# Optimization experiments

Measured on AMD Instinct MI355X. Metric: run time of the kernel, lower is better.

The kernel has to match this reference:

```python
import jax, jax.numpy as jnp
import numpy as np

N_NODES = 100000
N_EDGES = 1600000
DIM = 128
HEADS = 8
PHC = DIM // HEADS  # per-head channels = 16


def setup_inputs() -> dict:
    key = jax.random.key(0)
    k1, k2, k3, k4, k5 = jax.random.split(key, 5)
    nodes = jax.random.normal(k1, (N_NODES, DIM), dtype=jnp.float32)
    senders = jax.random.randint(k2, (N_EDGES,), 0, N_NODES, dtype=jnp.int32)
    receivers = jax.random.randint(k3, (N_EDGES,), 0, N_NODES, dtype=jnp.int32)
    # VarianceScaling(fan_avg, uniform) ~ limit = sqrt(3/fan_avg)
    lim_w = np.sqrt(3.0 / DIM)
    W = jax.random.uniform(k4, (DIM, DIM), minval=-lim_w, maxval=lim_w, dtype=jnp.float32)
    b = jnp.zeros((DIM,), dtype=jnp.float32)
    lim_a = np.sqrt(3.0 * 2.0 / (2 * PHC + 1))
    attn_w = jax.random.uniform(k5, (2 * PHC, 1), minval=-lim_a, maxval=lim_a, dtype=jnp.float32)
    attn_b = jnp.zeros((1,), dtype=jnp.float32)
    return {"nodes": nodes, "senders": senders, "receivers": receivers,
            "W": W, "b": b, "attn_w": attn_w, "attn_b": attn_b}


def reference(nodes, senders, receivers, W, b, attn_w, attn_b):
    n = nodes.shape[0]
    # linear transform + split heads: [N, H, PHC]
    nt = (nodes @ W + b).reshape(n, HEADS, PHC)
    sent = nt[senders]      # [E, H, PHC] gather
    recv = nt[receivers]    # [E, H, PHC] gather
    # attention logits: Linear(1) over leaky_relu(concat(q,k)) -> [E, H, 1]
    qk = jax.nn.leaky_relu(jnp.concatenate([sent, recv], axis=-1), negative_slope=0.2)
    logits = qk @ attn_w + attn_b  # [E, H, 1]
    # segment softmax over edges grouped by receiver node
    seg_max = jax.ops.segment_max(logits, receivers, num_segments=n)  # [N, H, 1]
    exp = jnp.exp(logits - seg_max[receivers])
    denom = jax.ops.segment_sum(exp, receivers, num_segments=n)  # [N, H, 1]
    alpha = exp / denom[receivers]
    # weighted scatter-sum of sender features
    out = jax.ops.segment_sum(sent * alpha, receivers, num_segments=n)  # [N, H, PHC]
    return out.reshape(n, -1)  # concat=True -> [N, DIM]
```

## Files before the change

### kernel.cpp

```cpp
#include <hip/hip_runtime.h>

#define DIM 128
#define HEADS 8
#define PHC 16

#define BSHIFT 6
#define BNODES 64
#define CAP 1408
#define NBMAX 1600

typedef __bf16 bf16x4 __attribute__((ext_vector_type(4)));
typedef __bf16 bf16x8 __attribute__((ext_vector_type(8)));
typedef float  f32x4  __attribute__((ext_vector_type(4)));

__device__ inline unsigned short f2bf(float x) {
  unsigned int u = __float_as_uint(x);
  unsigned int r = (u + 0x7FFF + ((u >> 16) & 1)) >> 16;
  return (unsigned short)r;
}

__global__ __launch_bounds__(256) void k_prepw(
    const float* __restrict__ W, __bf16* __restrict__ Wh,
    __bf16* __restrict__ Wl, int* __restrict__ gCursor, int NB) {
  const int tuple = blockIdx.x * 256 + threadIdx.x;
  if (tuple < NB) gCursor[tuple] = 0;
  const int ln = tuple & 15;
  const int lg = (tuple >> 4) & 3;
  const int cg = (tuple >> 6) & 7;
  const int kt = tuple >> 9;
  const int col = (cg << 4) + ln;
  bf16x8 h, l;
#pragma unroll
  for (int e = 0; e < 8; ++e) {
    int k = (kt << 5) + ((e >> 2) << 4) + (lg << 2) + (e & 3);
    float wv = W[k * DIM + col];
    __bf16 hh = (__bf16)wv;
    h[e] = hh;
    l[e] = (__bf16)(wv - (float)hh);
  }
  *(bf16x8*)(Wh + tuple * 8) = h;
  *(bf16x8*)(Wl + tuple * 8) = l;
}

#define GROWS 64

__global__ __launch_bounds__(256, 3) void k_gemm_scatter(
    const float* __restrict__ A, const __bf16* __restrict__ Wh,
    const __bf16* __restrict__ Wl, const float* __restrict__ bias,
    const float* __restrict__ attn_w, unsigned int* __restrict__ nt_t,
    float* __restrict__ s_exp_t, const int* __restrict__ send,
    const int* __restrict__ recv, int* __restrict__ gCursor,
    unsigned int* __restrict__ pairs, int E, int NB, int nScat, int n) {
  __shared__ __align__(16) float smemF[GROWS * DIM];

  if (blockIdx.x < nScat) {
    int* cnt = (int*)smemF;
    int* cur = cnt + NBMAX;
    const int t = threadIdx.x;
    for (int i = t; i < NB; i += 256) cnt[i] = 0;
    __syncthreads();
    const int e0 = blockIdx.x * 8192;
    const int e1 = min(e0 + 8192, E);
    for (int i = e0 + t; i < e1; i += 256)
      atomicAdd(&cnt[recv[i] >> BSHIFT], 1);
    __syncthreads();
    for (int i = t; i < NB; i += 256) {
      int c = cnt[i];
      cur[i] = i * CAP + (c ? atomicAdd(&gCursor[i], c) : 0);
    }
    __syncthreads();
    for (int i = e0 + t; i < e1; i += 256) {
      int r = recv[i];
      int b = r >> BSHIFT;
      int p = atomicAdd(&cur[b], 1);
      if (p - b * CAP < CAP)
        pairs[p] = (unsigned int)send[i] | ((unsigned int)(r & (BNODES - 1)) << 17);
    }
    return;
  }

  __bf16* Ah = (__bf16*)smemF;
  __bf16* Al = Ah + GROWS * DIM;
  const int t    = threadIdx.x;
  const int row0 = (blockIdx.x - nScat) * GROWS;
  const int lane = t & 63;
  const int w    = t >> 6;
  const int lg   = lane >> 4;
  const int ln   = lane & 15;

  float4 av[8];
  {
    const float4* A4 = (const float4*)(A + (size_t)row0 * DIM);
    const int lim = min(GROWS, n - row0) * (DIM / 4);
#pragma unroll
    for (int j = 0; j < 8; ++j) {
      int i = t + j * 256;
      av[j] = (i < lim) ? A4[i] : make_float4(0.f, 0.f, 0.f, 0.f);
    }
  }

#pragma unroll
  for (int j = 0; j < 8; ++j) {
    int i = t + j * 256;
    int r = i >> 5, c4 = i & 31;
    int ktc = c4 >> 3, lgc = c4 & 3, ehi = (c4 >> 2) & 1;
    int unit = (r << 4) + (((ktc << 2) + lgc) ^ (r & 15));
    int ei = (unit << 3) + (ehi << 2);
    float x0 = av[j].x, x1 = av[j].y, x2 = av[j].z, x3 = av[j].w;
    __bf16 h0 = (__bf16)x0, h1 = (__bf16)x1, h2 = (__bf16)x2, h3 = (__bf16)x3;
    bf16x4 hv = {h0, h1, h2, h3};
    bf16x4 lv = {(__bf16)(x0 - (float)h0), (__bf16)(x1 - (float)h1),
                 (__bf16)(x2 - (float)h2), (__bf16)(x3 - (float)h3)};
    *(bf16x4*)(Ah + ei) = hv;
    *(bf16x4*)(Al + ei) = lv;
  }

  f32x4 acc[4][2];
  {
    const float b0 = bias[(w << 5) + ln];
    const float b1 = bias[(w << 5) + 16 + ln];
#pragma unroll
    for (int rt = 0; rt < 4; ++rt) {
      acc[rt][0] = (f32x4){b0, b0, b0, b0};
      acc[rt][1] = (f32x4){b1, b1, b1, b1};
    }
  }
  __syncthreads();

  const int cg0 = w << 1;
#pragma unroll
  for (int kt = 0; kt < 4; ++kt) {
    bf16x8 Bh0, Bl0, Bh1, Bl1;
    {
      int i0 = ((((kt << 3) + cg0) << 2) + lg) * 16 + ln;
      int i1 = ((((kt << 3) + cg0 + 1) << 2) + lg) * 16 + ln;
      Bh0 = *(const bf16x8*)(Wh + (i0 << 3));
      Bl0 = *(const bf16x8*)(Wl + (i0 << 3));
      Bh1 = *(const bf16x8*)(Wh + (i1 << 3));
      Bl1 = *(const bf16x8*)(Wl + (i1 << 3));
    }
    bf16x8 ah[4], al[4];
#pragma unroll
    for (int rt = 0; rt < 4; ++rt) {
      int m = (rt << 4) + ln;
      int u = (m << 4) + (((kt << 2) + lg) ^ (m & 15));
      ah[rt] = *(const bf16x8*)(Ah + (u << 3));
      al[rt] = *(const bf16x8*)(Al + (u << 3));
    }
#pragma unroll
    for (int rt = 0; rt < 4; ++rt) {
      acc[rt][0] = __builtin_amdgcn_mfma_f32_16x16x32_bf16(ah[rt], Bh0, acc[rt][0], 0, 0, 0);
      acc[rt][0] = __builtin_amdgcn_mfma_f32_16x16x32_bf16(ah[rt], Bl0, acc[rt][0], 0, 0, 0);
      acc[rt][0] = __builtin_amdgcn_mfma_f32_16x16x32_bf16(al[rt], Bh0, acc[rt][0], 0, 0, 0);
      acc[rt][1] = __builtin_amdgcn_mfma_f32_16x16x32_bf16(ah[rt], Bh1, acc[rt][1], 0, 0, 0);
      acc[rt][1] = __builtin_amdgcn_mfma_f32_16x16x32_bf16(ah[rt], Bl1, acc[rt][1], 0, 0, 0);
      acc[rt][1] = __builtin_amdgcn_mfma_f32_16x16x32_bf16(al[rt], Bh1, acc[rt][1], 0, 0, 0);
    }
  }

  __syncthreads();

#pragma unroll
  for (int rt = 0; rt < 4; ++rt)
#pragma unroll
    for (int ct = 0; ct < 2; ++ct) {
      int colx = ((w << 5) + (ct << 4) + ln) ^ ((lg & 1) << 4);
#pragma unroll
      for (int r = 0; r < 4; ++r) {
        int rowl = (rt << 4) + (lg << 2) + r;
        smemF[(rowl << 7) + colx] = acc[rt][ct][r];
      }
    }

  {
    const float aw = attn_w[ln];
#pragma unroll
    for (int rt = 0; rt < 4; ++rt)
#pragma unroll
      for (int ct = 0; ct < 2; ++ct) {
        const int head = (w << 1) + ct;
#pragma unroll
        for (int r = 0; r < 4; ++r) {
          float v = acc[rt][ct][r];
          float p = (v > 0.f ? v : 0.2f * v) * aw;
          p += __shfl_xor(p, 1);
          p += __shfl_xor(p, 2);
          p += __shfl_xor(p, 4);
          p += __shfl_xor(p, 8);
          if (ln == 0) {
            int row = row0 + (rt << 4) + (lg << 2) + r;
            if (row < n) s_exp_t[(size_t)head * n + row] = __expf(p);
          }
        }
      }
  }
  __syncthreads();

  {
    const int nrow = min(GROWS, n - row0);
    const int r = t >> 2;
    const int q = t & 3;
    if (r < nrow) {
#pragma unroll
      for (int j = 0; j < 8; ++j) {
        int c4 = (j << 2) + q;
        int c4s = c4 ^ (((r >> 2) & 1) << 2);
        f32x4 v = *(const f32x4*)(smemF + (r << 7) + (c4s << 2));
        unsigned int lo = (unsigned int)f2bf(v[0]) | ((unsigned int)f2bf(v[1]) << 16);
        unsigned int hi = (unsigned int)f2bf(v[2]) | ((unsigned int)f2bf(v[3]) << 16);
        ((uint2*)nt_t)[((size_t)j * n + row0 + r) * 4 + q] = make_uint2(lo, hi);
      }
    }
  }
}

__global__ __launch_bounds__(256) void k_aggbuild(
    const unsigned int* __restrict__ pairs, const int* __restrict__ gCursor,
    const unsigned int* __restrict__ nt_t, const float* __restrict__ s_exp_t,
    float* __restrict__ out, int n) {
  __shared__ unsigned int buf[CAP];
  __shared__ int csr_l[CAP];
  __shared__ int hist[BNODES], offl[BNODES], curl[BNODES];
  const int b = blockIdx.x >> 3;
  const int h = blockIdx.x & 7;
  const int t = threadIdx.x;
  const int base = b * CAP;
  const int bsize = min(gCursor[b], CAP);

  for (int i = t; i < bsize; i += 256)
    buf[i] = __builtin_nontemporal_load(&pairs[base + i]);
  if (t < BNODES) hist[t] = 0;
  __syncthreads();
  for (int i = t; i < bsize; i += 256)
    atomicAdd(&hist[(buf[i] >> 17) & (BNODES - 1)], 1);
  __syncthreads();
  if (t < 64) {
    int v = hist[t];
    int x = v;
#pragma unroll
    for (int off = 1; off < 64; off <<= 1) {
      int y = __shfl_up(x, off);
      if (t >= off) x += y;
    }
    offl[t] = x - v;
    curl[t] = x - v;
  }
  __syncthreads();
  for (int i = t; i < bsize; i += 256) {
    unsigned int v = buf[i];
    int p = atomicAdd(&curl[(v >> 17) & (BNODES - 1)], 1);
    csr_l[p] = (int)(v & 0x1FFFF);
  }
  __syncthreads();

  const int nl = t >> 2;
  const int q  = t & 3;
  const int node = (b << BSHIFT) + nl;
  const int deg = hist[nl];
  const int eoff = offl[nl];
  const uint2* nt2 = (const uint2*)nt_t;
  const float* sp = s_exp_t + (size_t)h * n;
  const size_t pb4 = (size_t)h * n * 4;

  f32x4 a = {0.f, 0.f, 0.f, 0.f};
  float den = 0.f;
  for (int j = 0; j < deg; j += 4) {
    bool ok1 = (j + 1) < deg, ok2 = (j + 2) < deg, ok3 = (j + 3) < deg;
    int s0 = csr_l[eoff + j];
    int s1 = csr_l[ok1 ? (eoff + j + 1) : eoff];
    int s2 = csr_l[ok2 ? (eoff + j + 2) : eoff];
    int s3 = csr_l[ok3 ? (eoff + j + 3) : eoff];
    float w0 = sp[s0];
    float w1 = ok1 ? sp[s1] : 0.f;
    float w2 = ok2 ? sp[s2] : 0.f;
    float w3 = ok3 ? sp[s3] : 0.f;
    uint2 q0 = nt2[pb4 + s0 * 4 + q];
    uint2 q1 = nt2[pb4 + s1 * 4 + q];
    uint2 q2 = nt2[pb4 + s2 * 4 + q];
    uint2 q3 = nt2[pb4 + s3 * 4 + q];
    den += (w0 + w1) + (w2 + w3);
    a.x = fmaf(w0, __uint_as_float(q0.x << 16),
          fmaf(w1, __uint_as_float(q1.x << 16),
          fmaf(w2, __uint_as_float(q2.x << 16),
          fmaf(w3, __uint_as_float(q3.x << 16), a.x))));
    a.y = fmaf(w0, __uint_as_float(q0.x & 0xFFFF0000u),
          fmaf(w1, __uint_as_float(q1.x & 0xFFFF0000u),
          fmaf(w2, __uint_as_float(q2.x & 0xFFFF0000u),
          fmaf(w3, __uint_as_float(q3.x & 0xFFFF0000u), a.y))));
    a.z = fmaf(w0, __uint_as_float(q0.y << 16),
          fmaf(w1, __uint_as_float(q1.y << 16),
          fmaf(w2, __uint_as_float(q2.y << 16),
          fmaf(w3, __uint_as_float(q3.y << 16), a.z))));
    a.w = fmaf(w0, __uint_as_float(q0.y & 0xFFFF0000u),
          fmaf(w1, __uint_as_float(q1.y & 0xFFFF0000u),
          fmaf(w2, __uint_as_float(q2.y & 0xFFFF0000u),
          fmaf(w3, __uint_as_float(q3.y & 0xFFFF0000u), a.w))));
  }
  if (node < n) {
    const float inv = (deg > 0) ? 1.0f / den : 0.f;
    f32x4 o = {a.x * inv, a.y * inv, a.z * inv, a.w * inv};
    __builtin_nontemporal_store(
        o, (f32x4*)out + (size_t)node * 32 + (h << 2) + q);
  }
}

extern "C" void kernel_launch(void* const* d_in, const int* in_sizes, int n_in,
                              void* d_out, int out_size, void* d_ws, size_t ws_size,
                              hipStream_t stream) {
  const float* nodes   = (const float*)d_in[0];
  const int*   senders = (const int*)d_in[1];
  const int*   recvs   = (const int*)d_in[2];
  const float* W       = (const float*)d_in[3];
  const float* bias    = (const float*)d_in[4];
  const float* attn_w  = (const float*)d_in[5];

  const int n = in_sizes[0] / DIM;
  const int E = in_sizes[1];
  const int NB = (n + BNODES - 1) >> BSHIFT;

  char* w = (char*)d_ws;
  auto align256 = [](size_t x) { return (x + 255) & ~(size_t)255; };
  size_t off = 0;
  unsigned int* nt_t = (unsigned int*)(w + off); off += align256((size_t)n * DIM * 2);
  float* s_exp_t = (float*)(w + off); off += align256((size_t)n * HEADS * 4);
  unsigned int* pairs = (unsigned int*)(w + off); off += align256((size_t)NB * CAP * 4);
  int* gCursor   = (int*)(w + off);   off += align256((size_t)NB * 4);
  __bf16* Wh     = (__bf16*)(w + off); off += align256((size_t)2048 * 8 * 2);
  __bf16* Wl     = (__bf16*)(w + off); off += align256((size_t)2048 * 8 * 2);
  (void)ws_size;

  k_prepw<<<8, 256, 0, stream>>>(W, Wh, Wl, gCursor, NB);
  const int nScat = (E + 8191) / 8192;
  const int ngemm = (n + GROWS - 1) / GROWS;
  k_gemm_scatter<<<nScat + ngemm, 256, 0, stream>>>(
      nodes, Wh, Wl, bias, attn_w, nt_t, s_exp_t,
      senders, recvs, gCursor, pairs, E, NB, nScat, n);
  k_aggbuild<<<NB * 8, 256, 0, stream>>>(pairs, gCursor, nt_t, s_exp_t,
                                         (float*)d_out, n);
}
```

Measured before the change: 294.0 us.

## Split CSR build into its own kernel and sort nodes by degree

The per-bucket local CSR construction (histogram, scan, scatter) used to be repeated by all 8 head blocks of a bucket. It now runs once per bucket in a new kernel that writes the CSR and packed per-node metadata to global memory. That metadata orders nodes by descending degree, so wavefront lanes get balanced loop trip counts in the aggregation kernel. The cost is an extra kernel launch plus a global write and read of the CSR buffer.

After: 305.4 us. 1.04x slower.

```diff
diff --git a/kernel.cpp b/kernel.cpp
--- a/kernel.cpp
+++ b/kernel.cpp
@@ -214,50 +214,72 @@
   }
 }
 
-__global__ __launch_bounds__(256) void k_aggbuild(
+__global__ __launch_bounds__(256) void k_buildcsr(
     const unsigned int* __restrict__ pairs, const int* __restrict__ gCursor,
-    const unsigned int* __restrict__ nt_t, const float* __restrict__ s_exp_t,
-    float* __restrict__ out, int n) {
+    int* __restrict__ csr_g, unsigned int* __restrict__ meta_g) {
   __shared__ unsigned int buf[CAP];
+  __shared__ int hist[BNODES], curl[BNODES];
+  __shared__ unsigned int slotmeta[BNODES];
+  const int b = blockIdx.x;
+  const int t = threadIdx.x;
+  const int base = b * CAP;
+  const int bsize = min(gCursor[b], CAP);
+
+  for (int i = t; i < bsize; i += 256) buf[i] = pairs[base + i];
+  if (t < BNODES) hist[t] = 0;
+  __syncthreads();
+  for (int i = t; i < bsize; i += 256)
+    atomicAdd(&hist[(buf[i] >> 17) & (BNODES - 1)], 1);
+  __syncthreads();
+  if (t < 64) {
+    int v = hist[t];
+    int x = v;
+#pragma unroll
+    for (int off = 1; off < 64; off <<= 1) {
+      int y = __shfl_up(x, off);
+      if (t >= off) x += y;
+    }
+    int e = x - v;
+    curl[t] = e;
+    int rank = 0;
+    for (int j = 0; j < 64; ++j) {
+      int dj = hist[j];
+      rank += (dj > v) || (dj == v && j < t);
+    }
+    slotmeta[rank] = ((unsigned int)e << 17) | ((unsigned int)v << 6) |
+                     (unsigned int)t;
+  }
+  __syncthreads();
+  if (t < 64) meta_g[(b << 6) + t] = slotmeta[t];
+  for (int i = t; i < bsize; i += 256) {
+    unsigned int v = buf[i];
+    int p = atomicAdd(&curl[(v >> 17) & (BNODES - 1)], 1);
+    csr_g[base + p] = (int)(v & 0x1FFFF);
+  }
+}
+
+__global__ __launch_bounds__(256) void k_agg(
+    const int* __restrict__ csr_g, const int* __restrict__ gCursor,
+    const unsigned int* __restrict__ meta_g, const unsigned int* __restrict__ nt_t,
+    const float* __restrict__ s_exp_t, float* __restrict__ out, int n) {
   __shared__ int csr_l[CAP];
-  __shared__ int hist[BNODES], offl[BNODES], curl[BNODES];
+  __shared__ unsigned int smeta[BNODES];
   const int b = blockIdx.x >> 3;
   const int h = blockIdx.x & 7;
   const int t = threadIdx.x;
-  const int base = b * CAP;
   const int bsize = min(gCursor[b], CAP);
 
   for (int i = t; i < bsize; i += 256)
-    buf[i] = __builtin_nontemporal_load(&pairs[base + i]);
-  if (t < BNODES) hist[t] = 0;
-  __syncthreads();
-  for (int i = t; i < bsize; i += 256)
-    atomicAdd(&hist[(buf[i] >> 17) & (BNODES - 1)], 1);
-  __syncthreads();
-  if (t < 64) {
-    int v = hist[t];
-    int x = v;
-#pragma unroll
-    for (int off = 1; off < 64; off <<= 1) {
-      int y = __shfl_up(x, off);
-      if (t >= off) x += y;
-    }
-    offl[t] = x - v;
-    curl[t] = x - v;
-  }
-  __syncthreads();
-  for (int i = t; i < bsize; i += 256) {
-    unsigned int v = buf[i];
-    int p = atomicAdd(&curl[(v >> 17) & (BNODES - 1)], 1);
-    csr_l[p] = (int)(v & 0x1FFFF);
-  }
+    csr_l[i] = __builtin_nontemporal_load(&csr_g[b * CAP + i]);
+  if (t < BNODES) smeta[t] = meta_g[(b << 6) + t];
   __syncthreads();
 
   const int nl = t >> 2;
   const int q  = t & 3;
-  const int node = (b << BSHIFT) + nl;
-  const int deg = hist[nl];
-  const int eoff = offl[nl];
+  const unsigned int m = smeta[nl];
+  const int node = (b << BSHIFT) + (int)(m & 63);
+  const int deg  = (int)((m >> 6) & 0x7FF);
+  const int eoff = (int)(m >> 17);
   const uint2* nt2 = (const uint2*)nt_t;
   const float* sp = s_exp_t + (size_t)h * n;
   const size_t pb4 = (size_t)h * n * 4;
@@ -324,6 +346,8 @@
   unsigned int* nt_t = (unsigned int*)(w + off); off += align256((size_t)n * DIM * 2);
   float* s_exp_t = (float*)(w + off); off += align256((size_t)n * HEADS * 4);
   unsigned int* pairs = (unsigned int*)(w + off); off += align256((size_t)NB * CAP * 4);
+  int* csr_g     = (int*)(w + off);   off += align256((size_t)NB * CAP * 4);
+  unsigned int* meta_g = (unsigned int*)(w + off); off += align256((size_t)NB * 64 * 4);
   int* gCursor   = (int*)(w + off);   off += align256((size_t)NB * 4);
   __bf16* Wh     = (__bf16*)(w + off); off += align256((size_t)2048 * 8 * 2);
   __bf16* Wl     = (__bf16*)(w + off); off += align256((size_t)2048 * 8 * 2);
@@ -335,6 +359,7 @@
   k_gemm_scatter<<<nScat + ngemm, 256, 0, stream>>>(
       nodes, Wh, Wl, bias, attn_w, nt_t, s_exp_t,
       senders, recvs, gCursor, pairs, E, NB, nScat, n);
-  k_aggbuild<<<NB * 8, 256, 0, stream>>>(pairs, gCursor, nt_t, s_exp_t,
-                                         (float*)d_out, n);
-}
+  k_buildcsr<<<NB, 256, 0, stream>>>(pairs, gCursor, csr_g, meta_g);
+  k_agg<<<NB * 8, 256, 0, stream>>>(csr_g, gCursor, meta_g, nt_t, s_exp_t,
+                                    (float*)d_out, n);
+}
```
